# Kernel tuning notes

Hardware: AMD Instinct MI355X
Metric: run time of the kernel (lower is better)

The kernel has to match this reference:

```python
import jax, jax.numpy as jnp
import numpy as np

B, S, D = 4, 2048, 2048   # batch, seq, hidden
E, F, K = 8, 1024, 2      # experts, expert ffn dim, top-k
SF = 1024                 # shared-expert ffn dim
EPS = 1e-6


def setup_inputs() -> dict:
    key = jax.random.key(0)
    ks = jax.random.split(key, 9)
    g = lambda k, shape, scale: (jax.random.normal(k, shape, jnp.float32) * scale)
    return {
        "x": g(ks[0], (B, S, D), 1.0),
        "rms_weight": jnp.ones((D,), jnp.float32),
        "router_w": g(ks[1], (D, E), 0.02),
        "w_gate": g(ks[2], (E, D, F), 0.02),
        "w_up": g(ks[3], (E, D, F), 0.02),
        "w_down": g(ks[4], (E, F, D), 0.02),
        "sw_gate": g(ks[5], (D, SF), 0.02),
        "sw_up": g(ks[6], (D, SF), 0.02),
        "sw_down": g(ks[7], (SF, D), 0.02),
    }


def _rmsnorm(x, w, eps=EPS):
    var = jnp.mean(x * x, axis=-1, keepdims=True)
    return x * jax.lax.rsqrt(var + eps) * w


def reference(x, rms_weight, router_w, w_gate, w_up, w_down, sw_gate, sw_up, sw_down):
    b, s, d = x.shape
    e = router_w.shape[1]
    h = _rmsnorm(x, rms_weight)
    ht = h.reshape(-1, d)                      # [T, D] tokens
    t = ht.shape[0]

    # Router: softmax over experts, top-k, renormalize selected weights
    logits = ht @ router_w                     # [T, E]
    probs = jax.nn.softmax(logits, axis=-1)
    topv, topi = jax.lax.top_k(probs, K)       # [T, K]
    topv = topv / jnp.sum(topv, axis=-1, keepdims=True)
    # dense [T, E] combine weights (zero for non-selected experts)
    w_dense = jnp.zeros((t, e), ht.dtype).at[jnp.arange(t)[:, None], topi].set(topv)

    # Expert SwiGLU MLPs (grouped GEMM expressed densely over experts)
    g = jnp.einsum('td,edf->tef', ht, w_gate)  # [T, E, F]
    u = jnp.einsum('td,edf->tef', ht, w_up)
    eo = jnp.einsum('tef,efd->ted', jax.nn.silu(g) * u, w_down)  # [T, E, D]
    moe = jnp.einsum('te,ted->td', w_dense, eo)                   # weighted combine

    # Shared expert (SwiGLU)
    sh = (jax.nn.silu(ht @ sw_gate) * (ht @ sw_up)) @ sw_down

    return (moe + sh).reshape(b, s, d)
```

## Files before the change

### kernel.cpp

```cpp
#include <hip/hip_runtime.h>
#include <stdint.h>

#define T_TOK 8192
#define DDIM  2048
#define NEXP  8
#define FDIM  1024
#define CAP   25600
#define NT_M  200
#define BK    64

typedef __bf16 bf16x8 __attribute__((ext_vector_type(8)));
typedef float  f32x4  __attribute__((ext_vector_type(4)));

typedef const __attribute__((address_space(1))) uint32_t* as1_u32;
typedef __attribute__((address_space(3))) uint32_t* as3_u32;

__device__ __forceinline__ void gload16(const void* g, void* l) {
  __builtin_amdgcn_global_load_lds((as1_u32)g, (as3_u32)l, 16, 0, 0);
}
__device__ __forceinline__ float bf2f(uint16_t u) {
  union { uint32_t i; float f; } v; v.i = ((uint32_t)u) << 16; return v.f;
}
__device__ __forceinline__ uint16_t f2bf(float f) {
  union { float f; uint32_t i; } v; v.f = f;
  uint32_t i = v.i;
  i += 0x7FFFu + ((i >> 16) & 1u);
  return (uint16_t)(i >> 16);
}

__global__ __launch_bounds__(256) void k_rms_router(
    const float* __restrict__ x, const float* __restrict__ rmsw,
    const float* __restrict__ router_w, uint16_t* __restrict__ h,
    int* __restrict__ topi, float* __restrict__ topw, int* __restrict__ counts)
{
  int t = blockIdx.x, tid = threadIdx.x;
  int lane = tid & 63, wv = tid >> 6;
  const float* xr = x + (size_t)t * DDIM;
  float4 x0 = ((const float4*)xr)[tid * 2];
  float4 x1 = ((const float4*)xr)[tid * 2 + 1];
  float4 w0 = ((const float4*)rmsw)[tid * 2];
  float4 w1 = ((const float4*)rmsw)[tid * 2 + 1];
  float xv[8] = {x0.x, x0.y, x0.z, x0.w, x1.x, x1.y, x1.z, x1.w};
  float wv8[8] = {w0.x, w0.y, w0.z, w0.w, w1.x, w1.y, w1.z, w1.w};
  float ss = 0.f;
  #pragma unroll
  for (int j = 0; j < 8; j++) ss += xv[j] * xv[j];
  #pragma unroll
  for (int m = 32; m >= 1; m >>= 1) ss += __shfl_xor(ss, m, 64);
  __shared__ float rs[4];
  __shared__ float sscale;
  if (lane == 0) rs[wv] = ss;
  __syncthreads();
  if (tid == 0) sscale = rsqrtf((rs[0] + rs[1] + rs[2] + rs[3]) * (1.0f / DDIM) + 1e-6f);
  __syncthreads();
  float scale = sscale;
  float hv[8];
  #pragma unroll
  for (int j = 0; j < 8; j++) hv[j] = xv[j] * scale * wv8[j];
  ushort4 h0, h1;
  h0.x = f2bf(hv[0]); h0.y = f2bf(hv[1]); h0.z = f2bf(hv[2]); h0.w = f2bf(hv[3]);
  h1.x = f2bf(hv[4]); h1.y = f2bf(hv[5]); h1.z = f2bf(hv[6]); h1.w = f2bf(hv[7]);
  ((ushort4*)(h + (size_t)t * DDIM))[tid * 2]     = h0;
  ((ushort4*)(h + (size_t)t * DDIM))[tid * 2 + 1] = h1;

  float lp[8] = {0, 0, 0, 0, 0, 0, 0, 0};
  const float* rwm = router_w + (size_t)tid * 8 * NEXP;
  #pragma unroll
  for (int j = 0; j < 8; j++) {
    float4 a = ((const float4*)(rwm + j * NEXP))[0];
    float4 b = ((const float4*)(rwm + j * NEXP))[1];
    float hj = hv[j];
    lp[0] += hj * a.x; lp[1] += hj * a.y; lp[2] += hj * a.z; lp[3] += hj * a.w;
    lp[4] += hj * b.x; lp[5] += hj * b.y; lp[6] += hj * b.z; lp[7] += hj * b.w;
  }
  #pragma unroll
  for (int m = 32; m >= 1; m >>= 1) {
    #pragma unroll
    for (int e = 0; e < 8; e++) lp[e] += __shfl_xor(lp[e], m, 64);
  }
  __shared__ float rl[4][8];
  if (lane == 0) {
    #pragma unroll
    for (int e = 0; e < 8; e++) rl[wv][e] = lp[e];
  }
  __syncthreads();
  if (tid == 0) {
    float lg[8];
    #pragma unroll
    for (int e = 0; e < 8; e++) lg[e] = rl[0][e] + rl[1][e] + rl[2][e] + rl[3][e];
    int i0 = 0;
    for (int e = 1; e < 8; e++) if (lg[e] > lg[i0]) i0 = e;
    int i1 = (i0 == 0) ? 1 : 0;
    for (int e = 0; e < 8; e++) if (e != i0 && lg[e] > lg[i1]) i1 = e;
    float p0 = 1.f / (1.f + expf(lg[i1] - lg[i0]));
    topi[t * 2] = i0; topi[t * 2 + 1] = i1;
    topw[t * 2] = p0; topw[t * 2 + 1] = 1.f - p0;
    atomicAdd(&counts[i0], 1);
    atomicAdd(&counts[i1], 1);
  }
}

__global__ void k_offsets(const int* __restrict__ counts, int* __restrict__ off) {
  if (threadIdx.x == 0 && blockIdx.x == 0) {
    int o = 0;
    for (int e = 0; e < NEXP; e++) { off[e] = o; o += (counts[e] + 127) & ~127; }
    off[8] = o;
    off[9] = o + T_TOK;
  }
}

__global__ __launch_bounds__(256) void k_scatter(
    const int* __restrict__ topi, const float* __restrict__ topw,
    const int* __restrict__ off, int* __restrict__ cursor,
    int* __restrict__ tokslot, float* __restrict__ wtrow)
{
  int idx = blockIdx.x * 256 + threadIdx.x;
  if (idx < T_TOK * 2) {
    int t = idx >> 1, k = idx & 1;
    int e = topi[idx];
    int slot = atomicAdd(&cursor[e], 1);
    int row = off[e] + slot;
    tokslot[row] = t * 4 + k;
    wtrow[row] = topw[idx];
  } else {
    int t = idx - T_TOK * 2;
    int row = off[8] + t;
    tokslot[row] = t * 4 + 2;
    wtrow[row] = 1.0f;
  }
}

__global__ __launch_bounds__(256) void k_tr_df(
    const float* __restrict__ wg, const float* __restrict__ wu,
    const float* __restrict__ sg, const float* __restrict__ su,
    uint16_t* __restrict__ wgT, uint16_t* __restrict__ wuT,
    uint16_t* __restrict__ sgT, uint16_t* __restrict__ suT)
{
  __shared__ float tile[32][33];
  int z = blockIdx.z;
  const float* src; uint16_t* dst;
  if (z < 8)       { src = wg + (size_t)z * DDIM * FDIM;       dst = wgT + (size_t)z * FDIM * DDIM; }
  else if (z < 16) { src = wu + (size_t)(z - 8) * DDIM * FDIM; dst = wuT + (size_t)(z - 8) * FDIM * DDIM; }
  else if (z == 16){ src = sg; dst = sgT; }
  else             { src = su; dst = suT; }
  int c0 = blockIdx.x * 32, r0 = blockIdx.y * 32;
  int tx = threadIdx.x & 31, ty = threadIdx.x >> 5;
  #pragma unroll
  for (int i = 0; i < 4; i++)
    tile[ty + 8 * i][tx] = src[(size_t)(r0 + ty + 8 * i) * FDIM + c0 + tx];
  __syncthreads();
  #pragma unroll
  for (int i = 0; i < 4; i++)
    dst[(size_t)(c0 + ty + 8 * i) * DDIM + r0 + tx] = f2bf(tile[tx][ty + 8 * i]);
}

__global__ __launch_bounds__(256) void k_tr_fd(
    const float* __restrict__ wd, const float* __restrict__ sd,
    uint16_t* __restrict__ wdT, uint16_t* __restrict__ sdT)
{
  __shared__ float tile[32][33];
  int z = blockIdx.z;
  const float* src; uint16_t* dst;
  if (z < 8) { src = wd + (size_t)z * FDIM * DDIM; dst = wdT + (size_t)z * DDIM * FDIM; }
  else       { src = sd; dst = sdT; }
  int c0 = blockIdx.x * 32, r0 = blockIdx.y * 32;
  int tx = threadIdx.x & 31, ty = threadIdx.x >> 5;
  #pragma unroll
  for (int i = 0; i < 4; i++)
    tile[ty + 8 * i][tx] = src[(size_t)(r0 + ty + 8 * i) * DDIM + c0 + tx];
  __syncthreads();
  #pragma unroll
  for (int i = 0; i < 4; i++)
    dst[(size_t)(c0 + ty + 8 * i) * FDIM + r0 + tx] = f2bf(tile[tx][ty + 8 * i]);
}

#define BUFA(c) (ldsu + (size_t)(c) * 16384)
#define BUFB(c) (ldsu + 8192 + (size_t)(c) * 16384)

#define STAGE8(T, C) do {                                                     \
  _Pragma("unroll") for (int i_ = 0; i_ < 4; i_++) {                          \
    int G_ = w * 256 + i_ * 64 + lane;                                        \
    gload16(aSrc[i_] + (size_t)(T) * BK, BUFA(C) + G_ * 8);                   \
    gload16(bSrc[i_] + (size_t)(T) * BK, BUFB(C) + G_ * 8);                   \
  } } while (0)

#define COMPUTE_TILE(curA, curB) do {                                         \
  _Pragma("unroll") for (int ks_ = 0; ks_ < 2; ks_++) {                       \
    int ce_ = ks_ * 32 + ((lane >> 4) << 3);                                  \
    bf16x8 av_[4], bv_[4];                                                    \
    _Pragma("unroll") for (int m_ = 0; m_ < 4; m_++) {                        \
      int rr_ = wr * 64 + m_ * 16 + (lane & 15);                              \
      av_[m_] = *(const bf16x8*)((curA) + rr_ * 64 + (ce_ ^ ((rr_ & 7) << 3))); \
    }                                                                         \
    _Pragma("unroll") for (int n_ = 0; n_ < 4; n_++) {                        \
      int rr_ = wc * 64 + n_ * 16 + (lane & 15);                              \
      bv_[n_] = *(const bf16x8*)((curB) + rr_ * 64 + (ce_ ^ ((rr_ & 7) << 3))); \
    }                                                                         \
    __builtin_amdgcn_s_setprio(1);                                            \
    _Pragma("unroll") for (int m_ = 0; m_ < 4; m_++)                          \
    _Pragma("unroll") for (int n_ = 0; n_ < 4; n_++)                          \
      acc[m_][n_] = __builtin_amdgcn_mfma_f32_16x16x32_bf16(av_[m_], bv_[n_], acc[m_][n_], 0, 0, 0); \
    __builtin_amdgcn_s_setprio(0);                                            \
  } } while (0)

__global__ __launch_bounds__(256, 2) void k_stage1(
    const uint16_t* __restrict__ h, const uint16_t* __restrict__ wgT,
    const uint16_t* __restrict__ wuT, const uint16_t* __restrict__ sgT,
    const uint16_t* __restrict__ suT, const int* __restrict__ off,
    const int* __restrict__ tokslot, uint16_t* __restrict__ A_int)
{
  __shared__ __align__(16) uint16_t ldsu[32768];

  int row0 = blockIdx.y * 128;
  int end = off[9];
  if (row0 >= end) return;
  int e = 0;
  #pragma unroll 1
  for (; e < 9; e++) if (row0 >= off[e] && row0 < off[e + 1]) break;
  const uint16_t* bg = (e < NEXP) ? wgT + (size_t)e * FDIM * DDIM : sgT;
  const uint16_t* bu = (e < NEXP) ? wuT + (size_t)e * FDIM * DDIM : suT;
  int f0 = blockIdx.x * 64;

  int tid = threadIdx.x, lane = tid & 63, w = tid >> 6;
  int wr = w & 1, wc = w >> 1;

  const uint16_t* aSrc[4];
  const uint16_t* bSrc[4];
  #pragma unroll
  for (int i = 0; i < 4; i++) {
    int G = w * 256 + i * 64 + lane;
    int r = G >> 3, sl = G & 7;
    int gl = sl ^ (r & 7);
    int ts = tokslot[row0 + r];
    int tok = ts < 0 ? 0 : (ts >> 2);
    aSrc[i] = h + (size_t)tok * DDIM + gl * 8;
    int b = r >> 4;
    int fc = f0 + ((b >> 1) << 4) + (r & 15);
    const uint16_t* wbase = (b & 1) ? bu : bg;
    bSrc[i] = wbase + (size_t)fc * DDIM + gl * 8;
  }

  f32x4 acc[4][4] = {};
  const int NT = DDIM / BK;

  STAGE8(0, 0);
  __syncthreads();

  #pragma unroll 1
  for (int t = 0; t < NT; ++t) {
    int cur = t & 1;
    if (t + 1 < NT) STAGE8(t + 1, cur ^ 1);
    const uint16_t* curA = BUFA(cur);
    const uint16_t* curB = BUFB(cur);
    COMPUTE_TILE(curA, curB);
    __syncthreads();
  }

  #pragma unroll
  for (int m = 0; m < 4; m++) {
    #pragma unroll
    for (int p = 0; p < 2; p++) {
      #pragma unroll
      for (int r = 0; r < 4; r++) {
        int row = row0 + wr * 64 + m * 16 + ((lane >> 4) << 2) + r;
        int col = f0 + wc * 32 + p * 16 + (lane & 15);
        float g = acc[m][2 * p][r];
        float u = acc[m][2 * p + 1][r];
        float a = (g / (1.f + expf(-g))) * u;
        A_int[(size_t)row * FDIM + col] = f2bf(a);
      }
    }
  }
}

__global__ __launch_bounds__(256, 2) void k_stage2(
    const uint16_t* __restrict__ A_int, const uint16_t* __restrict__ wdT,
    const uint16_t* __restrict__ sdT, const int* __restrict__ off,
    const int* __restrict__ tokslot, const float* __restrict__ wtrow,
    uint16_t* __restrict__ eo, float* __restrict__ out)
{
  __shared__ __align__(16) uint16_t ldsu[32768];

  int row0 = blockIdx.y * 128;
  int end = off[9];
  if (row0 >= end) return;
  int e = 0;
  #pragma unroll 1
  for (; e < 9; e++) if (row0 >= off[e] && row0 < off[e + 1]) break;
  const uint16_t* bw = (e < NEXP) ? wdT + (size_t)e * DDIM * FDIM : sdT;
  int d0 = blockIdx.x * 128;

  int tid = threadIdx.x, lane = tid & 63, w = tid >> 6;
  int wr = w & 1, wc = w >> 1;

  const uint16_t* aSrc[4];
  const uint16_t* bSrc[4];
  #pragma unroll
  for (int i = 0; i < 4; i++) {
    int G = w * 256 + i * 64 + lane;
    int r = G >> 3, sl = G & 7;
    int gl = sl ^ (r & 7);
    aSrc[i] = A_int + (size_t)(row0 + r) * FDIM + gl * 8;
    bSrc[i] = bw + (size_t)(d0 + r) * FDIM + gl * 8;
  }

  f32x4 acc[4][4] = {};
  const int NT = FDIM / BK;

  STAGE8(0, 0);
  __syncthreads();

  #pragma unroll 1
  for (int t = 0; t < NT; ++t) {
    int cur = t & 1;
    if (t + 1 < NT) STAGE8(t + 1, cur ^ 1);
    const uint16_t* curA = BUFA(cur);
    const uint16_t* curB = BUFB(cur);
    COMPUTE_TILE(curA, curB);
    __syncthreads();
  }

  #pragma unroll
  for (int m = 0; m < 4; m++) {
    #pragma unroll
    for (int r = 0; r < 4; r++) {
      int grow = row0 + wr * 64 + m * 16 + ((lane >> 4) << 2) + r;
      int ts = tokslot[grow];
      if (ts < 0) continue;
      int tok = ts >> 2, slot = ts & 3;
      if (slot == 2) {
        size_t obase = (size_t)tok * DDIM;
        #pragma unroll
        for (int n = 0; n < 4; n++) {
          int col = d0 + wc * 64 + n * 16 + (lane & 15);
          out[obase + col] = acc[m][n][r];
        }
      } else {
        float wt = wtrow[grow];
        size_t obase = ((size_t)tok * 2 + slot) * DDIM;
        #pragma unroll
        for (int n = 0; n < 4; n++) {
          int col = d0 + wc * 64 + n * 16 + (lane & 15);
          eo[obase + col] = f2bf(acc[m][n][r] * wt);
        }
      }
    }
  }
}

__global__ __launch_bounds__(256) void k_final(
    const uint16_t* __restrict__ eo, float* __restrict__ out)
{
  int tok = blockIdx.x;
  int col = threadIdx.x * 8;
  const uint16_t* e0 = eo + ((size_t)tok * 2) * DDIM + col;
  const uint16_t* e1 = eo + ((size_t)tok * 2 + 1) * DDIM + col;
  float* op = out + (size_t)tok * DDIM + col;
  ushort4 a0 = *(const ushort4*)(e0);
  ushort4 a1 = *(const ushort4*)(e0 + 4);
  ushort4 b0 = *(const ushort4*)(e1);
  ushort4 b1 = *(const ushort4*)(e1 + 4);
  float4 s0 = *(const float4*)(op);
  float4 s1 = *(const float4*)(op + 4);
  float4 o0, o1;
  o0.x = s0.x + bf2f(a0.x) + bf2f(b0.x);
  o0.y = s0.y + bf2f(a0.y) + bf2f(b0.y);
  o0.z = s0.z + bf2f(a0.z) + bf2f(b0.z);
  o0.w = s0.w + bf2f(a0.w) + bf2f(b0.w);
  o1.x = s1.x + bf2f(a1.x) + bf2f(b1.x);
  o1.y = s1.y + bf2f(a1.y) + bf2f(b1.y);
  o1.z = s1.z + bf2f(a1.z) + bf2f(b1.z);
  o1.w = s1.w + bf2f(a1.w) + bf2f(b1.w);
  *(float4*)(op) = o0;
  *(float4*)(op + 4) = o1;
}

extern "C" void kernel_launch(void* const* d_in, const int* in_sizes, int n_in,
                              void* d_out, int out_size, void* d_ws, size_t ws_size,
                              hipStream_t stream) {
  (void)in_sizes; (void)n_in; (void)out_size;
  const float* x    = (const float*)d_in[0];
  const float* rmsw = (const float*)d_in[1];
  const float* rtw  = (const float*)d_in[2];
  const float* wg   = (const float*)d_in[3];
  const float* wu   = (const float*)d_in[4];
  const float* wd   = (const float*)d_in[5];
  const float* sg   = (const float*)d_in[6];
  const float* su   = (const float*)d_in[7];
  const float* sd   = (const float*)d_in[8];
  float* out = (float*)d_out;

  char* base = (char*)d_ws;
  size_t off_b = 0;
  auto place = [&](size_t bytes) { size_t r = off_b; off_b += (bytes + 255) & ~(size_t)255; return r; };
  size_t o_topi    = place((size_t)T_TOK * 2 * 4);
  size_t o_topw    = place((size_t)T_TOK * 2 * 4);
  size_t o_counts  = place(64);
  size_t o_offs    = place(64);
  size_t o_cursor  = place(64);
  size_t o_tokslot = place((size_t)CAP * 4);
  size_t o_wtrow   = place((size_t)CAP * 4);
  size_t o_h   = place((size_t)T_TOK * DDIM * 2);
  size_t o_wgT = place((size_t)NEXP * FDIM * DDIM * 2);
  size_t o_wuT = place((size_t)NEXP * FDIM * DDIM * 2);
  size_t o_sgT = place((size_t)FDIM * DDIM * 2);
  size_t o_suT = place((size_t)FDIM * DDIM * 2);
  size_t o_wdT = place((size_t)NEXP * DDIM * FDIM * 2);
  size_t o_sdT = place((size_t)DDIM * FDIM * 2);
  size_t o_Ai  = place((size_t)CAP * FDIM * 2);
  size_t o_eo  = o_h;
  size_t NEED = off_b;
  if (ws_size < NEED) return;

  int*      topi    = (int*)(base + o_topi);
  float*    topw    = (float*)(base + o_topw);
  int*      counts  = (int*)(base + o_counts);
  int*      offs    = (int*)(base + o_offs);
  int*      cursor  = (int*)(base + o_cursor);
  int*      tokslot = (int*)(base + o_tokslot);
  float*    wtrow   = (float*)(base + o_wtrow);
  uint16_t* h       = (uint16_t*)(base + o_h);
  uint16_t* wgT     = (uint16_t*)(base + o_wgT);
  uint16_t* wuT     = (uint16_t*)(base + o_wuT);
  uint16_t* sgT     = (uint16_t*)(base + o_sgT);
  uint16_t* suT     = (uint16_t*)(base + o_suT);
  uint16_t* wdT     = (uint16_t*)(base + o_wdT);
  uint16_t* sdT     = (uint16_t*)(base + o_sdT);
  uint16_t* Ai      = (uint16_t*)(base + o_Ai);
  uint16_t* eo      = (uint16_t*)(base + o_eo);

  hipMemsetAsync(counts, 0, 64, stream);
  hipMemsetAsync(cursor, 0, 64, stream);
  hipMemsetAsync(tokslot, 0xFF, (size_t)CAP * 4, stream);

  k_tr_df<<<dim3(FDIM / 32, DDIM / 32, 18), 256, 0, stream>>>(wg, wu, sg, su, wgT, wuT, sgT, suT);
  k_tr_fd<<<dim3(DDIM / 32, FDIM / 32, 9),  256, 0, stream>>>(wd, sd, wdT, sdT);

  k_rms_router<<<T_TOK, 256, 0, stream>>>(x, rmsw, rtw, h, topi, topw, counts);
  k_offsets<<<1, 64, 0, stream>>>(counts, offs);
  k_scatter<<<(T_TOK * 3) / 256, 256, 0, stream>>>(topi, topw, offs, cursor, tokslot, wtrow);

  k_stage1<<<dim3(FDIM / 64, NT_M), 256, 0, stream>>>(h, wgT, wuT, sgT, suT, offs, tokslot, Ai);
  k_stage2<<<dim3(DDIM / 128, NT_M), 256, 0, stream>>>(Ai, wdT, sdT, offs, tokslot, wtrow, eo, out);
  k_final<<<T_TOK, 256, 0, stream>>>(eo, out);
}
```

Baseline: 745.8 us.

## Remap GEMM blocks across XCDs and use one wave per token in router

The stage1 and stage2 grouped-GEMM kernels now remap their flat block index so that consecutive tiles sharing weight and row panels land on the same XCD. The intent is better L2 reuse on the multi-die MI355X. The RMSNorm/router kernel now gives each token to one 64-lane wave instead of a 256-thread block, which removes the shared-memory reductions and __syncthreads. The cost is more per-thread registers and strided router weight loads, and the remap assumes the grid size divides evenly by 8.

```diff
diff --git a/kernel.cpp b/kernel.cpp
--- a/kernel.cpp
+++ b/kernel.cpp
@@ -8,6 +8,9 @@
 #define CAP   25600
 #define NT_M  200
 #define BK    64
+#define GXT   16
+#define NBLK  (GXT * NT_M)
+#define CPX   (NBLK / 8)
 
 typedef __bf16 bf16x8 __attribute__((ext_vector_type(8)));
 typedef float  f32x4  __attribute__((ext_vector_type(4)));
@@ -33,66 +36,62 @@
     const float* __restrict__ router_w, uint16_t* __restrict__ h,
     int* __restrict__ topi, float* __restrict__ topw, int* __restrict__ counts)
 {
-  int t = blockIdx.x, tid = threadIdx.x;
-  int lane = tid & 63, wv = tid >> 6;
+  int wv = threadIdx.x >> 6, lane = threadIdx.x & 63;
+  int t = blockIdx.x * 4 + wv;
   const float* xr = x + (size_t)t * DDIM;
-  float4 x0 = ((const float4*)xr)[tid * 2];
-  float4 x1 = ((const float4*)xr)[tid * 2 + 1];
-  float4 w0 = ((const float4*)rmsw)[tid * 2];
-  float4 w1 = ((const float4*)rmsw)[tid * 2 + 1];
-  float xv[8] = {x0.x, x0.y, x0.z, x0.w, x1.x, x1.y, x1.z, x1.w};
-  float wv8[8] = {w0.x, w0.y, w0.z, w0.w, w1.x, w1.y, w1.z, w1.w};
+
+  float4 xv[8], wv8[8];
+  #pragma unroll
+  for (int j = 0; j < 8; j++) {
+    xv[j]  = ((const float4*)xr)[j * 64 + lane];
+    wv8[j] = ((const float4*)rmsw)[j * 64 + lane];
+  }
   float ss = 0.f;
   #pragma unroll
-  for (int j = 0; j < 8; j++) ss += xv[j] * xv[j];
+  for (int j = 0; j < 8; j++)
+    ss += xv[j].x * xv[j].x + xv[j].y * xv[j].y + xv[j].z * xv[j].z + xv[j].w * xv[j].w;
   #pragma unroll
   for (int m = 32; m >= 1; m >>= 1) ss += __shfl_xor(ss, m, 64);
-  __shared__ float rs[4];
-  __shared__ float sscale;
-  if (lane == 0) rs[wv] = ss;
-  __syncthreads();
-  if (tid == 0) sscale = rsqrtf((rs[0] + rs[1] + rs[2] + rs[3]) * (1.0f / DDIM) + 1e-6f);
-  __syncthreads();
-  float scale = sscale;
-  float hv[8];
-  #pragma unroll
-  for (int j = 0; j < 8; j++) hv[j] = xv[j] * scale * wv8[j];
-  ushort4 h0, h1;
-  h0.x = f2bf(hv[0]); h0.y = f2bf(hv[1]); h0.z = f2bf(hv[2]); h0.w = f2bf(hv[3]);
-  h1.x = f2bf(hv[4]); h1.y = f2bf(hv[5]); h1.z = f2bf(hv[6]); h1.w = f2bf(hv[7]);
-  ((ushort4*)(h + (size_t)t * DDIM))[tid * 2]     = h0;
-  ((ushort4*)(h + (size_t)t * DDIM))[tid * 2 + 1] = h1;
+  float scale = rsqrtf(ss * (1.0f / DDIM) + 1e-6f);
+
+  float hv[8][4];
+  #pragma unroll
+  for (int j = 0; j < 8; j++) {
+    hv[j][0] = xv[j].x * scale * wv8[j].x;
+    hv[j][1] = xv[j].y * scale * wv8[j].y;
+    hv[j][2] = xv[j].z * scale * wv8[j].z;
+    hv[j][3] = xv[j].w * scale * wv8[j].w;
+    ushort4 hw;
+    hw.x = f2bf(hv[j][0]); hw.y = f2bf(hv[j][1]);
+    hw.z = f2bf(hv[j][2]); hw.w = f2bf(hv[j][3]);
+    ((ushort4*)(h + (size_t)t * DDIM))[j * 64 + lane] = hw;
+  }
 
   float lp[8] = {0, 0, 0, 0, 0, 0, 0, 0};
-  const float* rwm = router_w + (size_t)tid * 8 * NEXP;
   #pragma unroll
   for (int j = 0; j < 8; j++) {
-    float4 a = ((const float4*)(rwm + j * NEXP))[0];
-    float4 b = ((const float4*)(rwm + j * NEXP))[1];
-    float hj = hv[j];
-    lp[0] += hj * a.x; lp[1] += hj * a.y; lp[2] += hj * a.z; lp[3] += hj * a.w;
-    lp[4] += hj * b.x; lp[5] += hj * b.y; lp[6] += hj * b.z; lp[7] += hj * b.w;
+    #pragma unroll
+    for (int c = 0; c < 4; c++) {
+      int d = (j * 64 + lane) * 4 + c;
+      const float* rw = router_w + (size_t)d * NEXP;
+      float4 a = ((const float4*)rw)[0];
+      float4 b = ((const float4*)rw)[1];
+      float hj = hv[j][c];
+      lp[0] += hj * a.x; lp[1] += hj * a.y; lp[2] += hj * a.z; lp[3] += hj * a.w;
+      lp[4] += hj * b.x; lp[5] += hj * b.y; lp[6] += hj * b.z; lp[7] += hj * b.w;
+    }
   }
   #pragma unroll
   for (int m = 32; m >= 1; m >>= 1) {
     #pragma unroll
     for (int e = 0; e < 8; e++) lp[e] += __shfl_xor(lp[e], m, 64);
   }
-  __shared__ float rl[4][8];
   if (lane == 0) {
-    #pragma unroll
-    for (int e = 0; e < 8; e++) rl[wv][e] = lp[e];
-  }
-  __syncthreads();
-  if (tid == 0) {
-    float lg[8];
-    #pragma unroll
-    for (int e = 0; e < 8; e++) lg[e] = rl[0][e] + rl[1][e] + rl[2][e] + rl[3][e];
     int i0 = 0;
-    for (int e = 1; e < 8; e++) if (lg[e] > lg[i0]) i0 = e;
+    for (int e = 1; e < 8; e++) if (lp[e] > lp[i0]) i0 = e;
     int i1 = (i0 == 0) ? 1 : 0;
-    for (int e = 0; e < 8; e++) if (e != i0 && lg[e] > lg[i1]) i1 = e;
-    float p0 = 1.f / (1.f + expf(lg[i1] - lg[i0]));
+    for (int e = 0; e < 8; e++) if (e != i0 && lp[e] > lp[i1]) i1 = e;
+    float p0 = 1.f / (1.f + expf(lp[i1] - lp[i0]));
     topi[t * 2] = i0; topi[t * 2 + 1] = i1;
     topw[t * 2] = p0; topw[t * 2 + 1] = 1.f - p0;
     atomicAdd(&counts[i0], 1);
@@ -176,6 +175,12 @@
 
 #define BUFA(c) (ldsu + (size_t)(c) * 16384)
 #define BUFB(c) (ldsu + 8192 + (size_t)(c) * 16384)
+
+#define XCD_REMAP()                                                            \
+  int flat_ = blockIdx.y * GXT + blockIdx.x;                                   \
+  int nf_ = (flat_ & 7) * CPX + (flat_ >> 3);                                  \
+  int bx = nf_ & (GXT - 1);                                                    \
+  int by = nf_ / GXT;
 
 #define STAGE8(T, C) do {                                                     \
   _Pragma("unroll") for (int i_ = 0; i_ < 4; i_++) {                          \
@@ -211,7 +216,8 @@
 {
   __shared__ __align__(16) uint16_t ldsu[32768];
 
-  int row0 = blockIdx.y * 128;
+  XCD_REMAP();
+  int row0 = by * 128;
   int end = off[9];
   if (row0 >= end) return;
   int e = 0;
@@ -219,7 +225,7 @@
   for (; e < 9; e++) if (row0 >= off[e] && row0 < off[e + 1]) break;
   const uint16_t* bg = (e < NEXP) ? wgT + (size_t)e * FDIM * DDIM : sgT;
   const uint16_t* bu = (e < NEXP) ? wuT + (size_t)e * FDIM * DDIM : suT;
-  int f0 = blockIdx.x * 64;
+  int f0 = bx * 64;
 
   int tid = threadIdx.x, lane = tid & 63, w = tid >> 6;
   int wr = w & 1, wc = w >> 1;
@@ -281,14 +287,15 @@
 {
   __shared__ __align__(16) uint16_t ldsu[32768];
 
-  int row0 = blockIdx.y * 128;
+  XCD_REMAP();
+  int row0 = by * 128;
   int end = off[9];
   if (row0 >= end) return;
   int e = 0;
   #pragma unroll 1
   for (; e < 9; e++) if (row0 >= off[e] && row0 < off[e + 1]) break;
   const uint16_t* bw = (e < NEXP) ? wdT + (size_t)e * DDIM * FDIM : sdT;
-  int d0 = blockIdx.x * 128;
+  int d0 = bx * 128;
 
   int tid = threadIdx.x, lane = tid & 63, w = tid >> 6;
   int wr = w & 1, wc = w >> 1;
@@ -436,11 +443,11 @@
   k_tr_df<<<dim3(FDIM / 32, DDIM / 32, 18), 256, 0, stream>>>(wg, wu, sg, su, wgT, wuT, sgT, suT);
   k_tr_fd<<<dim3(DDIM / 32, FDIM / 32, 9),  256, 0, stream>>>(wd, sd, wdT, sdT);
 
-  k_rms_router<<<T_TOK, 256, 0, stream>>>(x, rmsw, rtw, h, topi, topw, counts);
+  k_rms_router<<<T_TOK / 4, 256, 0, stream>>>(x, rmsw, rtw, h, topi, topw, counts);
   k_offsets<<<1, 64, 0, stream>>>(counts, offs);
   k_scatter<<<(T_TOK * 3) / 256, 256, 0, stream>>>(topi, topw, offs, cursor, tokslot, wtrow);
 
-  k_stage1<<<dim3(FDIM / 64, NT_M), 256, 0, stream>>>(h, wgT, wuT, sgT, suT, offs, tokslot, Ai);
-  k_stage2<<<dim3(DDIM / 128, NT_M), 256, 0, stream>>>(Ai, wdT, sdT, offs, tokslot, wtrow, eo, out);
+  k_stage1<<<dim3(GXT, NT_M), 256, 0, stream>>>(h, wgT, wuT, sgT, suT, offs, tokslot, Ai);
+  k_stage2<<<dim3(GXT, NT_M), 256, 0, stream>>>(Ai, wdT, sdT, offs, tokslot, wtrow, eo, out);
   k_final<<<T_TOK, 256, 0, stream>>>(eo, out);
 }
```

After: 746.0 us. No clear change (+0.0%).
